# Kernel tuning notes

Measured on AMD Instinct MI355X. Metric: run time of the kernel, lower is better.

Reference implementation:

```python
import jax, jax.numpy as jnp
import numpy as np

EMB = 768
HEADS = 12
B, N = 32, 1024


def setup_inputs() -> dict:
    key = jax.random.key(0)
    ks = jax.random.split(key, 7)
    s = 1.0 / np.sqrt(EMB)
    return {
        "x": jax.random.normal(ks[0], (B, N, EMB), dtype=jnp.float32),
        "Wq": jax.random.normal(ks[1], (EMB, EMB), dtype=jnp.float32) * s,
        "bq": jnp.zeros((EMB,), dtype=jnp.float32),
        "Wk": jax.random.normal(ks[2], (EMB, EMB), dtype=jnp.float32) * s,
        "bk": jnp.zeros((EMB,), dtype=jnp.float32),
        "Wv": jax.random.normal(ks[3], (EMB, EMB), dtype=jnp.float32) * s,
        "bv": jnp.zeros((EMB,), dtype=jnp.float32),
    }


def reference(x, Wq, bq, Wk, bk, Wv, bv):
    b, n, _ = x.shape
    h = HEADS
    e = EMB // h  # head dim
    # project and split heads: b n (h e) -> b h n e
    def split(t):
        return t.reshape(b, n, h, e).transpose(0, 2, 1, 3)
    q = split(x @ Wq + bq)
    k = split(x @ Wk + bk)
    v = split(x @ Wv + bv)
    # NOTE: scale is 1/sqrt(num_head), as in the original module
    wei = jnp.einsum('bhie,bhje->bhij', q, k) / jnp.sqrt(jnp.float32(h))
    # NOTE: softmax over dim=2 = query axis i (non-standard)
    wei = jax.nn.softmax(wei, axis=2)
    # dropout is identity in eval mode
    out = jnp.einsum('bhij,bhje->bhie', wei, v)
    return out.transpose(0, 2, 1, 3).reshape(b, n, h * e)
```

## Files before the change

kernel.cpp:

```cpp
#include <hip/hip_runtime.h>

#define EMB 768
#define NH 12
#define HD 64
#define BB 32
#define NN 1024
#define QSCALE 0.41647025f

typedef _Float16 h8 __attribute__((ext_vector_type(8)));
typedef _Float16 h4 __attribute__((ext_vector_type(4)));
typedef _Float16 h2 __attribute__((ext_vector_type(2)));
typedef float f4 __attribute__((ext_vector_type(4)));

static __device__ __forceinline__ f4 mfma16(h8 a, h8 b, f4 c) {
  return __builtin_amdgcn_mfma_f32_16x16x32_f16(a, b, c, 0, 0, 0);
}

static __device__ __forceinline__ h2 cvt_pk(float a, float b) {
  return __builtin_bit_cast(h2, __builtin_amdgcn_cvt_pkrtz(a, b));
}

static __device__ __forceinline__ float exp2a(float x) {
#if __has_builtin(__builtin_amdgcn_exp2f)
  return __builtin_amdgcn_exp2f(x);
#else
  float r;
  asm("v_exp_f32 %0, %1\n\ts_nop 1" : "=v"(r) : "v"(x));
  return r;
#endif
}

static __device__ __forceinline__ void gload16(const _Float16* g, _Float16* lds) {
  __builtin_amdgcn_global_load_lds(
      (const __attribute__((address_space(1))) void*)g,
      (__attribute__((address_space(3))) void*)lds, 16, 0, 0);
}

__global__ __launch_bounds__(256) void k_cvt(const float* __restrict__ X,
                                             _Float16* __restrict__ Xh, int n4) {
  int i = blockIdx.x * 256 + threadIdx.x;
  if (i >= n4) return;
  float4 v = ((const float4*)X)[i];
  h4 o = {(_Float16)v.x, (_Float16)v.y, (_Float16)v.z, (_Float16)v.w};
  ((h4*)Xh)[i] = o;
}

__global__ __launch_bounds__(256) void k_wt(const float* __restrict__ W0,
                                            const float* __restrict__ W1,
                                            const float* __restrict__ W2,
                                            _Float16* __restrict__ Wt) {
  const float* W = blockIdx.z == 0 ? W0 : (blockIdx.z == 1 ? W1 : W2);
  _Float16* dst = Wt + (size_t)blockIdx.z * EMB * EMB;
  __shared__ float tile[64][65];
  const int t = threadIdx.x;
  const int r0 = blockIdx.y * 64, c0 = blockIdx.x * 64;
  const int r = t >> 4, c4 = (t & 15) * 4;
#pragma unroll
  for (int i = 0; i < 4; ++i) {
    const float4 v = *(const float4*)&W[(size_t)(r0 + r + 16 * i) * EMB + c0 + c4];
    tile[r + 16 * i][c4 + 0] = v.x; tile[r + 16 * i][c4 + 1] = v.y;
    tile[r + 16 * i][c4 + 2] = v.z; tile[r + 16 * i][c4 + 3] = v.w;
  }
  __syncthreads();
  const int cc = t >> 2, rr = (t & 3) * 16;
#pragma unroll
  for (int half = 0; half < 2; ++half) {
    h8 o;
#pragma unroll
    for (int j = 0; j < 8; ++j) o[j] = (_Float16)tile[rr + half * 8 + j][cc];
    *(h8*)&dst[(size_t)(c0 + cc) * EMB + r0 + rr + half * 8] = o;
  }
}

__global__ __launch_bounds__(256) void k_projf(const _Float16* __restrict__ Xh,
                                               const _Float16* __restrict__ Wt,
                                               const float* __restrict__ bq,
                                               const float* __restrict__ bk,
                                               const float* __restrict__ bv,
                                               _Float16* __restrict__ Qw,
                                               _Float16* __restrict__ Kw,
                                               _Float16* __restrict__ Vtmp) {
  __shared__ _Float16 As[2][128 * 64];
  __shared__ _Float16 Bs[2][128 * 64];
  const int t = threadIdx.x;
  const int w = t >> 6, l = t & 63;
  const int wm = w >> 1, wn = w & 1;
  const int p = l & 15, g = l >> 4;
  const int by = blockIdx.x;
  const int m0 = blockIdx.y * 128;
  const int n0 = by * 128;

  f4 acc[4][4];
#pragma unroll
  for (int mf = 0; mf < 4; ++mf)
#pragma unroll
    for (int nf = 0; nf < 4; ++nf) acc[mf][nf] = f4{0.f, 0.f, 0.f, 0.f};

  const int lrow = l >> 3, lch = (l & 7) ^ (l >> 3);

#define STAGE(buf, k0)                                                            \
  {                                                                               \
    _Float16* ab = &As[buf][0];                                                   \
    _Float16* bb = &Bs[buf][0];                                                   \
    _Pragma("unroll") for (int i = 0; i < 4; ++i) {                               \
      const int seg = (w << 2) | i;                                               \
      const int grow = (seg << 3) | lrow;                                         \
      gload16(Xh + (size_t)(m0 + grow) * EMB + (k0) + lch * 8, ab + seg * 512);   \
      gload16(Wt + (size_t)(n0 + grow) * EMB + (k0) + lch * 8, bb + seg * 512);   \
    }                                                                             \
  }

  STAGE(0, 0)
  __syncthreads();

  int cur = 0;
  for (int kt = 0; kt < 12; ++kt) {
    if (kt + 1 < 12) STAGE(cur ^ 1, (kt + 1) * 64)
    const char* asb = (const char*)&As[cur][0];
    const char* bsb = (const char*)&Bs[cur][0];
#pragma unroll
    for (int ks = 0; ks < 2; ++ks) {
      h8 af[4], bf[4];
#pragma unroll
      for (int mf = 0; mf < 4; ++mf)
        af[mf] = *(const h8*)(asb + ((wm * 64 + mf * 16 + p) << 7) +
                              ((((ks << 2) | g) ^ (p & 7)) << 4));
#pragma unroll
      for (int nf = 0; nf < 4; ++nf)
        bf[nf] = *(const h8*)(bsb + ((wn * 64 + nf * 16 + p) << 7) +
                              ((((ks << 2) | g) ^ (p & 7)) << 4));
#pragma unroll
      for (int mf = 0; mf < 4; ++mf)
#pragma unroll
        for (int nf = 0; nf < 4; ++nf) acc[mf][nf] = mfma16(af[mf], bf[nf], acc[mf][nf]);
    }
    __syncthreads();
    cur ^= 1;
  }
#undef STAGE

  const int z = by / 6;
  const int nl0 = (by % 6) * 128;
  const float* bias = z == 0 ? bq : (z == 1 ? bk : bv);
  _Float16* Outz = z == 0 ? Qw : (z == 1 ? Kw : Vtmp);
  const float scale = z == 0 ? QSCALE : 1.0f;
#pragma unroll
  for (int nf = 0; nf < 4; ++nf) {
    const int C = nl0 + wn * 64 + nf * 16 + p;
    const float bvv = bias[C];
    const int h = C >> 6, e = C & 63;
#pragma unroll
    for (int mf = 0; mf < 4; ++mf) {
#pragma unroll
      for (int r = 0; r < 4; ++r) {
        const int R = m0 + wm * 64 + mf * 16 + g * 4 + r;
        const int b = R >> 10, tok = R & 1023;
        Outz[((size_t)(b * NH + h) * NN + tok) * HD + e] = (_Float16)((acc[mf][nf][r] + bvv) * scale);
      }
    }
  }
}

__global__ __launch_bounds__(256) void k_stats(const _Float16* __restrict__ Q,
                                               const _Float16* __restrict__ K,
                                               float* __restrict__ Lg, float* __restrict__ MT) {
  const int bh = blockIdx.x * 48 + (blockIdx.y >> 3);
  const int jt = blockIdx.y & 7;
  const int j0 = jt * 128;
  __shared__ _Float16 Ks[128][64];
  __shared__ _Float16 Qs[128][64];
  __shared__ float Lj[128];
  __shared__ float reds[2][128];
  __shared__ float MsSh;
  const _Float16* Qb = Q + (size_t)bh * NN * HD;
  const _Float16* Kb = K + (size_t)bh * NN * HD;
  const int t = threadIdx.x, w = t >> 6, l = t & 63;
  const int wi = w >> 1, wj = w & 1;
  const int p = l & 15, g = l >> 4;
  const int lr = t >> 3, tc = t & 7;
  char* ksb = (char*)&Ks[0][0];
  char* qsb = (char*)&Qs[0][0];
#pragma unroll
  for (int i = 0; i < 4; ++i)
    *(h8*)(ksb + ((lr + 32 * i) << 7) + ((tc ^ (lr & 7)) << 4)) =
        *(const h8*)&Kb[(size_t)(j0 + lr + 32 * i) * HD + tc * 8];
  if (t < 128) Lj[t] = 0.f;
  __syncthreads();

  for (int i0 = 0; i0 < NN; i0 += 128) {
#pragma unroll
    for (int i = 0; i < 4; ++i)
      *(h8*)(qsb + ((lr + 32 * i) << 7) + ((tc ^ (lr & 7)) << 4)) =
          *(const h8*)&Qb[(size_t)(i0 + lr + 32 * i) * HD + tc * 8];
    __syncthreads();
    f4 s[4][4];
#pragma unroll
    for (int mf = 0; mf < 4; ++mf)
#pragma unroll
      for (int nf = 0; nf < 4; ++nf) s[mf][nf] = f4{0.f, 0.f, 0.f, 0.f};
#pragma unroll
    for (int ks = 0; ks < 2; ++ks) {
      h8 af[4], bf[4];
#pragma unroll
      for (int mf = 0; mf < 4; ++mf)
        af[mf] = *(const h8*)(qsb + ((wi * 64 + mf * 16 + p) << 7) + ((((ks << 2) | g) ^ (p & 7)) << 4));
#pragma unroll
      for (int nf = 0; nf < 4; ++nf)
        bf[nf] = *(const h8*)(ksb + ((wj * 64 + nf * 16 + p) << 7) + ((((ks << 2) | g) ^ (p & 7)) << 4));
#pragma unroll
      for (int mf = 0; mf < 4; ++mf)
#pragma unroll
        for (int nf = 0; nf < 4; ++nf) s[mf][nf] = mfma16(af[mf], bf[nf], s[mf][nf]);
    }
#pragma unroll
    for (int nf = 0; nf < 4; ++nf) {
      float cs = 0.f;
#pragma unroll
      for (int mf = 0; mf < 4; ++mf)
#pragma unroll
        for (int r = 0; r < 4; ++r) cs += exp2a(s[mf][nf][r]);
      cs += __shfl_xor(cs, 16);
      cs += __shfl_xor(cs, 32);
      if (l < 16) reds[wi][wj * 64 + nf * 16 + l] = cs;
    }
    __syncthreads();
    if (t < 128) Lj[t] += reds[0][t] + reds[1][t];
    __syncthreads();
  }
  if (w == 0) {
    float mv = fmaxf(Lj[l], Lj[l + 64]);
#pragma unroll
    for (int d = 32; d; d >>= 1) mv = fmaxf(mv, __shfl_xor(mv, d));
    if (l == 0) { MsSh = __log2f(mv); MT[bh * 8 + jt] = MsSh; }
  }
  __syncthreads();
  const float msc = exp2a(-MsSh);
  if (t < 128) Lg[(size_t)bh * NN + j0 + t] = Lj[t] * msc;
}

__global__ __launch_bounds__(256) void k_vt(const _Float16* __restrict__ Vtmp,
                                            const float* __restrict__ Lg,
                                            _Float16* __restrict__ Vt) {
  const int bh = blockIdx.y, j0 = blockIdx.x * 64;
  __shared__ _Float16 tile[64][72];
  const _Float16* src = Vtmp + (size_t)bh * NN * HD;
  _Float16* dst = Vt + (size_t)bh * HD * NN;
  const int t = threadIdx.x;
  const int jr = t >> 3, e8 = (t & 7) * 8;
#pragma unroll
  for (int i = 0; i < 2; ++i) {
    const float inv = 1.0f / Lg[(size_t)bh * NN + j0 + jr + 32 * i];
    h8 v = *(const h8*)&src[(size_t)(j0 + jr + 32 * i) * HD + e8];
    h8 o;
#pragma unroll
    for (int j = 0; j < 8; ++j) o[j] = (_Float16)((float)v[j] * inv);
    *(h8*)&tile[jr + 32 * i][e8] = o;
  }
  __syncthreads();
  const int er = t >> 3, j8 = (t & 7) * 8;
#pragma unroll
  for (int i = 0; i < 2; ++i) {
    h8 o;
#pragma unroll
    for (int j = 0; j < 8; ++j) o[j] = tile[j8 + j][er + 32 * i];
    *(h8*)&dst[(size_t)(er + 32 * i) * NN + j0 + j8] = o;
  }
}

__global__ __launch_bounds__(256) void k_out(const _Float16* __restrict__ Q,
                                             const _Float16* __restrict__ K,
                                             const _Float16* __restrict__ Vt,
                                             const float* __restrict__ MT,
                                             float* __restrict__ Out) {
  const int bh = blockIdx.x * 48 + (blockIdx.y >> 2);
  const int i0 = (blockIdx.y & 3) * 256;
  const int b = bh / NH, h = bh % NH;
  __shared__ _Float16 Ks[2][32][64];
  __shared__ _Float16 Vts[2][64][32];
  __shared__ _Float16 Ps[4][2][32][32];
  const _Float16* Qb = Q + (size_t)bh * NN * HD;
  const _Float16* Kb = K + (size_t)bh * NN * HD;
  const _Float16* Vb = Vt + (size_t)bh * HD * NN;
  const int t = threadIdx.x, w = t >> 6, l = t & 63;
  const int p = l & 15, g = l >> 4;
  char* psb[2] = {(char*)&Ps[w][0][0][0], (char*)&Ps[w][1][0][0]};

  h8 bq[2][2][2];
#pragma unroll
  for (int it = 0; it < 2; ++it)
#pragma unroll
    for (int f = 0; f < 2; ++f)
#pragma unroll
      for (int ks = 0; ks < 2; ++ks)
        bq[it][f][ks] = *(const h8*)&Qb[(size_t)(i0 + it * 128 + w * 32 + f * 16 + p) * HD + ks * 32 + g * 8];

  f4 oacc[2][4][2];
#pragma unroll
  for (int it = 0; it < 2; ++it)
#pragma unroll
    for (int ef = 0; ef < 4; ++ef)
#pragma unroll
      for (int f = 0; f < 2; ++f) oacc[it][ef][f] = f4{0.f, 0.f, 0.f, 0.f};

  const int kr = t >> 3, kc = t & 7;
  const int vr = t >> 2, vc = t & 3;

  h8 kreg = *(const h8*)&Kb[(size_t)kr * HD + kc * 8];
  h8 vreg = *(const h8*)&Vb[(size_t)vr * NN + vc * 8];
  *(h8*)((char*)&Ks[0][0][0] + (kr << 7) + ((kc ^ (kr & 7)) << 4)) = kreg;
  *(h8*)((char*)&Vts[0][0][0] + (vr << 6) + ((vc ^ ((vr >> 1) & 3)) << 4)) = vreg;

  for (int jt4 = 0; jt4 < 8; ++jt4) {
    const float Mstar = MT[bh * 8 + jt4];
#pragma unroll
    for (int u = 0; u < 4; ++u) {
      const int jt = jt4 * 4 + u;
      const int cur = u & 1;
      char* ksb = (char*)&Ks[cur][0][0];
      char* vsb = (char*)&Vts[cur][0][0];
      __syncthreads();
      if (jt + 1 < 32) {
        const int j0n = (jt + 1) * 32;
        kreg = *(const h8*)&Kb[(size_t)(j0n + kr) * HD + kc * 8];
        vreg = *(const h8*)&Vb[(size_t)vr * NN + j0n + vc * 8];
      }

      h8 ak[2][2], av[4];
#pragma unroll
      for (int ks = 0; ks < 2; ++ks)
#pragma unroll
        for (int jf = 0; jf < 2; ++jf)
          ak[ks][jf] = *(const h8*)(ksb + ((jf * 16 + p) << 7) + ((((ks << 2) | g) ^ (p & 7)) << 4));
#pragma unroll
      for (int ef = 0; ef < 4; ++ef)
        av[ef] = *(const h8*)(vsb + ((ef * 16 + p) << 6) + ((g ^ ((p >> 1) & 3)) << 4));

#pragma unroll
      for (int it = 0; it < 2; ++it) {
        f4 s[2][2];
#pragma unroll
        for (int f = 0; f < 2; ++f)
#pragma unroll
          for (int jf = 0; jf < 2; ++jf) s[f][jf] = f4{-Mstar, -Mstar, -Mstar, -Mstar};
#pragma unroll
        for (int ks = 0; ks < 2; ++ks)
#pragma unroll
          for (int f = 0; f < 2; ++f)
#pragma unroll
            for (int jf = 0; jf < 2; ++jf) s[f][jf] = mfma16(ak[ks][jf], bq[it][f][ks], s[f][jf]);
#pragma unroll
        for (int f = 0; f < 2; ++f)
#pragma unroll
          for (int jf = 0; jf < 2; ++jf) {
            const f4 sv = s[f][jf];
            h2 lo = cvt_pk(exp2a(sv[0]), exp2a(sv[1]));
            h2 hi = cvt_pk(exp2a(sv[2]), exp2a(sv[3]));
            h4 pw; pw[0] = lo[0]; pw[1] = lo[1]; pw[2] = hi[0]; pw[3] = hi[1];
            *(h4*)(psb[it] + ((f * 16 + p) << 6) +
                   (((2 * jf + (g >> 1)) ^ ((p >> 1) & 3)) << 4) + ((g & 1) << 3)) = pw;
          }
      }
      asm volatile("s_waitcnt lgkmcnt(0)" ::: "memory");
      __builtin_amdgcn_sched_barrier(0);

#pragma unroll
      for (int it = 0; it < 2; ++it) {
        h8 bp[2];
#pragma unroll
        for (int f = 0; f < 2; ++f)
          bp[f] = *(const h8*)(psb[it] + ((f * 16 + p) << 6) + ((g ^ ((p >> 1) & 3)) << 4));
#pragma unroll
        for (int ef = 0; ef < 4; ++ef)
#pragma unroll
          for (int f = 0; f < 2; ++f) oacc[it][ef][f] = mfma16(av[ef], bp[f], oacc[it][ef][f]);
      }

      if (jt + 1 < 32) {
        *(h8*)((char*)&Ks[cur ^ 1][0][0] + (kr << 7) + ((kc ^ (kr & 7)) << 4)) = kreg;
        *(h8*)((char*)&Vts[cur ^ 1][0][0] + (vr << 6) + ((vc ^ ((vr >> 1) & 3)) << 4)) = vreg;
      }
    }
  }

#pragma unroll
  for (int it = 0; it < 2; ++it) {
#pragma unroll
    for (int f = 0; f < 2; ++f) {
      const int i = i0 + it * 128 + w * 32 + f * 16 + p;
#pragma unroll
      for (int ef = 0; ef < 4; ++ef) {
        float4 o4 = {oacc[it][ef][f][0], oacc[it][ef][f][1], oacc[it][ef][f][2], oacc[it][ef][f][3]};
        *(float4*)&Out[((size_t)b * NN + i) * EMB + h * HD + ef * 16 + 4 * g] = o4;
      }
    }
  }
}

extern "C" void kernel_launch(void* const* d_in, const int* in_sizes, int n_in,
                              void* d_out, int out_size, void* d_ws, size_t ws_size,
                              hipStream_t stream) {
  const float* X  = (const float*)d_in[0];
  const float* Wq = (const float*)d_in[1];
  const float* bq = (const float*)d_in[2];
  const float* Wk = (const float*)d_in[3];
  const float* bk = (const float*)d_in[4];
  const float* Wv = (const float*)d_in[5];
  const float* bv = (const float*)d_in[6];

  char* ws = (char*)d_ws;
  _Float16* Qw = (_Float16*)(ws);
  _Float16* Kw = (_Float16*)(ws + 50331648);
  _Float16* Vt = (_Float16*)(ws + 100663296);
  _Float16* Wt = (_Float16*)(ws + 150994944);
  float* Lg    = (float*)(ws + 154533888);
  float* MT    = (float*)(ws + 156106752);

  _Float16* Xh   = (_Float16*)d_out;
  _Float16* Vtmp = (_Float16*)((char*)d_out + 50331648);
  float* Out = (float*)d_out;

  k_cvt<<<dim3(6291456 / 256), 256, 0, stream>>>(X, Xh, 6291456);
  k_wt<<<dim3(12, 12, 3), 256, 0, stream>>>(Wq, Wk, Wv, Wt);
  k_projf<<<dim3(18, 256), 256, 0, stream>>>(Xh, Wt, bq, bk, bv, Qw, Kw, Vtmp);
  k_stats<<<dim3(8, 384), 256, 0, stream>>>(Qw, Kw, Lg, MT);
  k_vt<<<dim3(16, 384), 256, 0, stream>>>(Vtmp, Lg, Vt);
  k_out<<<dim3(8, 192), 256, 0, stream>>>(Qw, Kw, Vt, MT, Out);
}
```

Measured before the change: 397.3 us.

## Fuse V scaling/transpose into stats kernel and single-buffer projection GEMM

The V normalization and transpose kernel is merged into the column-stats kernel, which now scales V rows by their column-sum reciprocals from shared memory and writes the transposed Vt directly. This removes one launch and the round trip of the Lg array through global memory. The stats kernel now loads Q/K with direct global-to-LDS loads and reuses the same shared buffer for the V tile. The projection GEMM drops double buffering in favour of a single LDS stage. That cuts LDS use, possibly allowing more resident blocks, but exposes load latency because the loads no longer overlap the MFMAs.

New measurement: 399.9 us. Within noise of the previous version (+0.6%).

```diff
diff --git a/kernel.cpp b/kernel.cpp
--- a/kernel.cpp
+++ b/kernel.cpp
@@ -80,8 +80,8 @@
                                                _Float16* __restrict__ Qw,
                                                _Float16* __restrict__ Kw,
                                                _Float16* __restrict__ Vtmp) {
-  __shared__ _Float16 As[2][128 * 64];
-  __shared__ _Float16 Bs[2][128 * 64];
+  __shared__ _Float16 As[128 * 64];
+  __shared__ _Float16 Bs[128 * 64];
   const int t = threadIdx.x;
   const int w = t >> 6, l = t & 63;
   const int wm = w >> 1, wn = w & 1;
@@ -98,26 +98,18 @@
 
   const int lrow = l >> 3, lch = (l & 7) ^ (l >> 3);
 
-#define STAGE(buf, k0)                                                            \
-  {                                                                               \
-    _Float16* ab = &As[buf][0];                                                   \
-    _Float16* bb = &Bs[buf][0];                                                   \
-    _Pragma("unroll") for (int i = 0; i < 4; ++i) {                               \
-      const int seg = (w << 2) | i;                                               \
-      const int grow = (seg << 3) | lrow;                                         \
-      gload16(Xh + (size_t)(m0 + grow) * EMB + (k0) + lch * 8, ab + seg * 512);   \
-      gload16(Wt + (size_t)(n0 + grow) * EMB + (k0) + lch * 8, bb + seg * 512);   \
-    }                                                                             \
-  }
-
-  STAGE(0, 0)
-  __syncthreads();
-
-  int cur = 0;
   for (int kt = 0; kt < 12; ++kt) {
-    if (kt + 1 < 12) STAGE(cur ^ 1, (kt + 1) * 64)
-    const char* asb = (const char*)&As[cur][0];
-    const char* bsb = (const char*)&Bs[cur][0];
+    const int k0 = kt * 64;
+#pragma unroll
+    for (int i = 0; i < 4; ++i) {
+      const int seg = (w << 2) | i;
+      const int grow = (seg << 3) | lrow;
+      gload16(Xh + (size_t)(m0 + grow) * EMB + k0 + lch * 8, As + seg * 512);
+      gload16(Wt + (size_t)(n0 + grow) * EMB + k0 + lch * 8, Bs + seg * 512);
+    }
+    __syncthreads();
+    const char* asb = (const char*)&As[0];
+    const char* bsb = (const char*)&Bs[0];
 #pragma unroll
     for (int ks = 0; ks < 2; ++ks) {
       h8 af[4], bf[4];
@@ -135,9 +127,7 @@
         for (int nf = 0; nf < 4; ++nf) acc[mf][nf] = mfma16(af[mf], bf[nf], acc[mf][nf]);
     }
     __syncthreads();
-    cur ^= 1;
-  }
-#undef STAGE
+  }
 
   const int z = by / 6;
   const int nl0 = (by % 6) * 128;
@@ -163,35 +153,44 @@
 
 __global__ __launch_bounds__(256) void k_stats(const _Float16* __restrict__ Q,
                                                const _Float16* __restrict__ K,
-                                               float* __restrict__ Lg, float* __restrict__ MT) {
+                                               const _Float16* __restrict__ Vtmp,
+                                               float* __restrict__ MT,
+                                               _Float16* __restrict__ Vt) {
   const int bh = blockIdx.x * 48 + (blockIdx.y >> 3);
   const int jt = blockIdx.y & 7;
   const int j0 = jt * 128;
-  __shared__ _Float16 Ks[128][64];
-  __shared__ _Float16 Qs[128][64];
-  __shared__ float Lj[128];
-  __shared__ float reds[2][128];
-  __shared__ float MsSh;
+  __shared__ __align__(16) char SMEM[35080];
+  _Float16* Ks = (_Float16*)SMEM;
+  _Float16* Qs = (_Float16*)(SMEM + 16384);
+  float* Lj    = (float*)(SMEM + 32768);
+  float* reds  = (float*)(SMEM + 33280);
+  float* MsShp = (float*)(SMEM + 34312);
+  _Float16 (*Vtile)[72] = (_Float16(*)[72])SMEM;
   const _Float16* Qb = Q + (size_t)bh * NN * HD;
   const _Float16* Kb = K + (size_t)bh * NN * HD;
   const int t = threadIdx.x, w = t >> 6, l = t & 63;
   const int wi = w >> 1, wj = w & 1;
   const int p = l & 15, g = l >> 4;
-  const int lr = t >> 3, tc = t & 7;
-  char* ksb = (char*)&Ks[0][0];
-  char* qsb = (char*)&Qs[0][0];
-#pragma unroll
-  for (int i = 0; i < 4; ++i)
-    *(h8*)(ksb + ((lr + 32 * i) << 7) + ((tc ^ (lr & 7)) << 4)) =
-        *(const h8*)&Kb[(size_t)(j0 + lr + 32 * i) * HD + tc * 8];
+  const int lrow = l >> 3, lch = (l & 7) ^ (l >> 3);
+
+#pragma unroll
+  for (int i = 0; i < 4; ++i) {
+    const int seg = (w << 2) | i;
+    const int grow = (seg << 3) | lrow;
+    gload16(Kb + (size_t)(j0 + grow) * HD + lch * 8, Ks + seg * 512);
+  }
   if (t < 128) Lj[t] = 0.f;
   __syncthreads();
 
+  const char* ksb = (const char*)Ks;
+  const char* qsb = (const char*)Qs;
   for (int i0 = 0; i0 < NN; i0 += 128) {
 #pragma unroll
-    for (int i = 0; i < 4; ++i)
-      *(h8*)(qsb + ((lr + 32 * i) << 7) + ((tc ^ (lr & 7)) << 4)) =
-          *(const h8*)&Qb[(size_t)(i0 + lr + 32 * i) * HD + tc * 8];
+    for (int i = 0; i < 4; ++i) {
+      const int seg = (w << 2) | i;
+      const int grow = (seg << 3) | lrow;
+      gload16(Qb + (size_t)(i0 + grow) * HD + lch * 8, Qs + seg * 512);
+    }
     __syncthreads();
     f4 s[4][4];
 #pragma unroll
@@ -221,49 +220,45 @@
         for (int r = 0; r < 4; ++r) cs += exp2a(s[mf][nf][r]);
       cs += __shfl_xor(cs, 16);
       cs += __shfl_xor(cs, 32);
-      if (l < 16) reds[wi][wj * 64 + nf * 16 + l] = cs;
-    }
-    __syncthreads();
-    if (t < 128) Lj[t] += reds[0][t] + reds[1][t];
+      if (l < 16) reds[wi * 128 + wj * 64 + nf * 16 + l] = cs;
+    }
+    __syncthreads();
+    if (t < 128) Lj[t] += reds[t] + reds[128 + t];
     __syncthreads();
   }
   if (w == 0) {
     float mv = fmaxf(Lj[l], Lj[l + 64]);
 #pragma unroll
     for (int d = 32; d; d >>= 1) mv = fmaxf(mv, __shfl_xor(mv, d));
-    if (l == 0) { MsSh = __log2f(mv); MT[bh * 8 + jt] = MsSh; }
+    if (l == 0) { MsShp[0] = __log2f(mv); MT[bh * 8 + jt] = MsShp[0]; }
   }
   __syncthreads();
-  const float msc = exp2a(-MsSh);
-  if (t < 128) Lg[(size_t)bh * NN + j0 + t] = Lj[t] * msc;
-}
-
-__global__ __launch_bounds__(256) void k_vt(const _Float16* __restrict__ Vtmp,
-                                            const float* __restrict__ Lg,
-                                            _Float16* __restrict__ Vt) {
-  const int bh = blockIdx.y, j0 = blockIdx.x * 64;
-  __shared__ _Float16 tile[64][72];
-  const _Float16* src = Vtmp + (size_t)bh * NN * HD;
-  _Float16* dst = Vt + (size_t)bh * HD * NN;
-  const int t = threadIdx.x;
-  const int jr = t >> 3, e8 = (t & 7) * 8;
-#pragma unroll
-  for (int i = 0; i < 2; ++i) {
-    const float inv = 1.0f / Lg[(size_t)bh * NN + j0 + jr + 32 * i];
-    h8 v = *(const h8*)&src[(size_t)(j0 + jr + 32 * i) * HD + e8];
-    h8 o;
-#pragma unroll
-    for (int j = 0; j < 8; ++j) o[j] = (_Float16)((float)v[j] * inv);
-    *(h8*)&tile[jr + 32 * i][e8] = o;
-  }
-  __syncthreads();
-  const int er = t >> 3, j8 = (t & 7) * 8;
-#pragma unroll
-  for (int i = 0; i < 2; ++i) {
-    h8 o;
-#pragma unroll
-    for (int j = 0; j < 8; ++j) o[j] = tile[j8 + j][er + 32 * i];
-    *(h8*)&dst[(size_t)(er + 32 * i) * NN + j0 + j8] = o;
+  const float rmsc = exp2a(MsShp[0]);
+
+  const _Float16* Vb = Vtmp + (size_t)bh * NN * HD;
+  _Float16* Vo = Vt + (size_t)bh * HD * NN;
+  const int jr = t >> 3, c8 = (t & 7) * 8;
+#pragma unroll
+  for (int half = 0; half < 2; ++half) {
+#pragma unroll
+    for (int i = 0; i < 2; ++i) {
+      const int jl = half * 64 + jr + 32 * i;
+      const float inv = rmsc / Lj[jl];
+      h8 v = *(const h8*)&Vb[(size_t)(j0 + jl) * HD + c8];
+      h8 o;
+#pragma unroll
+      for (int j = 0; j < 8; ++j) o[j] = (_Float16)((float)v[j] * inv);
+      *(h8*)&Vtile[jr + 32 * i][c8] = o;
+    }
+    __syncthreads();
+#pragma unroll
+    for (int i = 0; i < 2; ++i) {
+      h8 o;
+#pragma unroll
+      for (int j = 0; j < 8; ++j) o[j] = Vtile[c8 + j][jr + 32 * i];
+      *(h8*)&Vo[(size_t)(jr + 32 * i) * NN + j0 + half * 64 + c8] = o;
+    }
+    __syncthreads();
   }
 }
 
@@ -412,8 +407,7 @@
   _Float16* Kw = (_Float16*)(ws + 50331648);
   _Float16* Vt = (_Float16*)(ws + 100663296);
   _Float16* Wt = (_Float16*)(ws + 150994944);
-  float* Lg    = (float*)(ws + 154533888);
-  float* MT    = (float*)(ws + 156106752);
+  float* MT    = (float*)(ws + 154533888);
 
   _Float16* Xh   = (_Float16*)d_out;
   _Float16* Vtmp = (_Float16*)((char*)d_out + 50331648);
@@ -422,7 +416,6 @@
   k_cvt<<<dim3(6291456 / 256), 256, 0, stream>>>(X, Xh, 6291456);
   k_wt<<<dim3(12, 12, 3), 256, 0, stream>>>(Wq, Wk, Wv, Wt);
   k_projf<<<dim3(18, 256), 256, 0, stream>>>(Xh, Wt, bq, bk, bv, Qw, Kw, Vtmp);
-  k_stats<<<dim3(8, 384), 256, 0, stream>>>(Qw, Kw, Lg, MT);
-  k_vt<<<dim3(16, 384), 256, 0, stream>>>(Vtmp, Lg, Vt);
+  k_stats<<<dim3(8, 384), 256, 0, stream>>>(Qw, Kw, Vtmp, MT, Vt);
   k_out<<<dim3(8, 192), 256, 0, stream>>>(Qw, Kw, Vt, MT, Out);
 }
```
